# Optimization experiments

Measured on AMD Instinct MI355X. Metric: run time of the kernel, lower is better.

The kernel has to match this reference:

```python
import jax, jax.numpy as jnp
import numpy as np

H = 8        # num_heads
LN_EPS = 1e-5
NEG = -1000000.0


def setup_inputs() -> dict:
    key = jax.random.key(0)
    ks = jax.random.split(key, 8)
    B, T, D = 4, 4096, 1024
    s = 1.0 / np.sqrt(D)
    x = jax.random.normal(ks[0], (B, T, D), dtype=jnp.float32)
    tmask = (jnp.arange(T) < (3 * T) // 4).astype(jnp.float32)
    src_mask = jnp.broadcast_to(tmask[None, :, None], (B, T, 1)).astype(jnp.float32)
    Wq = jax.random.normal(ks[1], (D, D), dtype=jnp.float32) * s
    Wk = jax.random.normal(ks[2], (D, D), dtype=jnp.float32) * s
    Wv = jax.random.normal(ks[3], (D, D), dtype=jnp.float32) * s
    bq = jnp.zeros((D,), jnp.float32)
    bk = jnp.zeros((D,), jnp.float32)
    bv = jnp.zeros((D,), jnp.float32)
    gamma = jnp.ones((D,), jnp.float32)
    beta = jnp.zeros((D,), jnp.float32)
    return {"x": x, "src_mask": src_mask, "Wq": Wq, "bq": bq, "Wk": Wk,
            "bk": bk, "Wv": Wv, "bv": bv, "gamma": gamma, "beta": beta}


def reference(x, src_mask, Wq, bq, Wk, bk, Wv, bv, gamma, beta):
    B, T, D = x.shape
    Dh = D // H
    # LayerNorm (same normed input feeds q, k, v)
    mu = jnp.mean(x, axis=-1, keepdims=True)
    var = jnp.mean(jnp.square(x - mu), axis=-1, keepdims=True)
    xn = (x - mu) * jax.lax.rsqrt(var + LN_EPS) * gamma + beta
    q = xn @ Wq + bq                               # [B,T,D]
    k = xn @ Wk + bk + (1.0 - src_mask) * NEG      # mask padded timesteps
    v = (xn @ Wv + bv) * src_mask                  # zero padded values
    q = jax.nn.softmax(q.reshape(B, T, H, Dh), axis=-1)   # over feature dim
    k = jax.nn.softmax(k.reshape(B, T, H, Dh), axis=1)    # over time dim
    v = v.reshape(B, T, H, Dh)
    # efficient/linear attention: O(T * Dh^2) per head
    att = jnp.einsum('bnhd,bnhl->bhdl', k, v)      # [B,H,Dh,Dh]
    y = jnp.einsum('bnhd,bhdl->bnhl', q, att).reshape(B, T, D)
    return x + y
```

## Files before the change

### kernel.cpp

```cpp
#include <hip/hip_runtime.h>
#include <stdint.h>


typedef unsigned short u16;
typedef __attribute__((ext_vector_type(8))) short bf16x8;
typedef __attribute__((ext_vector_type(4))) float f32x4;

__device__ u16 g_WT[3][1024 * 1024];
__device__ u16 g_xn[16777216];
__device__ u16 g_ekT[16777216];
__device__ u16 g_vvT[16777216];
__device__ float g_attp[8388608];
__device__ u16 g_attT[524288];
__device__ float g_Z[4096];

__device__ __forceinline__ float b2f(u16 u) {
  union { unsigned int i; float f; } c;
  c.i = ((unsigned int)u) << 16;
  return c.f;
}
__device__ __forceinline__ u16 f2b(float f) {
  union { float f; unsigned int i; } c;
  c.f = f;
  unsigned int r = c.i + 0x7fffu + ((c.i >> 16) & 1u);
  return (u16)(r >> 16);
}

__device__ __forceinline__ void gload16(const void* g, void* l) {
  __builtin_amdgcn_global_load_lds(
      reinterpret_cast<const __attribute__((address_space(1))) uint32_t*>(
          reinterpret_cast<uintptr_t>(g)),
      reinterpret_cast<__attribute__((address_space(3))) uint32_t*>(
          reinterpret_cast<uintptr_t>(l)),
      16, 0, 0);
}

__device__ __forceinline__ void stage128x32(const u16* g, int stride, char* lds,
                                            int wave, int lane) {
  const int r = wave * 32 + (lane >> 2);
  const int cb = (lane & 3) * 16;
  const char* gp = (const char*)g;
  gload16(gp + (size_t)r * stride * 2 + cb, lds + wave * 2048);
  gload16(gp + (size_t)(r + 16) * stride * 2 + cb, lds + wave * 2048 + 1024);
}

__device__ __forceinline__ bf16x8 frag_ld(const char* lds, int row, int lane) {
  return *(const bf16x8*)(lds + row * 64 + ((lane >> 4) * 16));
}

__device__ __forceinline__ void tile_mfma(const char* As, const char* Bs,
                                          f32x4 (&acc)[4][4], int wm, int wn,
                                          int lane) {
  bf16x8 af[4], bfr[4];
#pragma unroll
  for (int i = 0; i < 4; i++) af[i] = frag_ld(As, wm * 64 + i * 16 + (lane & 15), lane);
#pragma unroll
  for (int j = 0; j < 4; j++) bfr[j] = frag_ld(Bs, wn * 64 + j * 16 + (lane & 15), lane);
#pragma unroll
  for (int i = 0; i < 4; i++)
#pragma unroll
    for (int j = 0; j < 4; j++)
      acc[i][j] = __builtin_amdgcn_mfma_f32_16x16x32_bf16(af[i], bfr[j], acc[i][j], 0, 0, 0);
}

__device__ __forceinline__ void stageA256(char* buf, const u16* gsrc, int h,
                                          int wave, int lane) {
#pragma unroll
  for (int i = 0; i < 2; i++) {
    const int ib = i * 64 + wave * 8;
    const int rowb = (ib & 63) | ((ib & 64) << 1) | (h << 6);
    const int row = rowb + (lane >> 3);
    const int cc = (lane & 7) ^ (row & 7);
    gload16((const char*)gsrc + ((size_t)row * 1024 + cc * 8) * 2,
            buf + rowb * 128);
  }
}
__device__ __forceinline__ void stageB256(char* buf, const u16* gsrc, int h,
                                          int wave, int lane) {
#pragma unroll
  for (int i = 0; i < 2; i++) {
    const int ib = i * 64 + wave * 8;
    const int rowb = (ib & 31) | ((ib & 96) << 1) | (h << 5);
    const int row = rowb + (lane >> 3);
    const int cc = (lane & 7) ^ (row & 7);
    gload16((const char*)gsrc + ((size_t)row * 1024 + cc * 8) * 2,
            buf + rowb * 128);
  }
}
__device__ __forceinline__ bf16x8 fragS(const char* buf, int R, int ks, int lane) {
  const int q = lane >> 4;
  return *(const bf16x8*)(buf + R * 128 + ((((ks << 2) + q) ^ (R & 7)) << 4));
}

template <bool ST>
__device__ __forceinline__ void tile_r8(char* Ab, char* Bb, char* An, char* Bn,
                                        const u16* Agn, const u16* Bgn,
                                        f32x4 (&acc)[8][4], int wave, int lane,
                                        int wm, int wn) {
  bf16x8 a[4][2], bB[2][2][2];

#pragma unroll
  for (int rf = 0; rf < 4; rf++) {
    const int R = wm * 128 + rf * 16 + (lane & 15);
#pragma unroll
    for (int ks = 0; ks < 2; ks++) a[rf][ks] = fragS(Ab, R, ks, lane);
  }
#pragma unroll
  for (int cf = 0; cf < 2; cf++) {
    const int R = wn * 64 + cf * 16 + (lane & 15);
#pragma unroll
    for (int ks = 0; ks < 2; ks++) bB[0][cf][ks] = fragS(Bb, R, ks, lane);
  }
  if constexpr (ST) {
    stageA256(An, Agn, 0, wave, lane);
    stageB256(Bn, Bgn, 0, wave, lane);
    asm volatile("s_waitcnt vmcnt(4)" ::: "memory");
  } else {
    asm volatile("s_waitcnt vmcnt(0)" ::: "memory");
  }
  __builtin_amdgcn_s_barrier();
  asm volatile("s_waitcnt lgkmcnt(0)" ::: "memory");
  __builtin_amdgcn_sched_barrier(0);
  __builtin_amdgcn_s_setprio(1);
#pragma unroll
  for (int rf = 0; rf < 4; rf++)
#pragma unroll
    for (int cf = 0; cf < 2; cf++)
#pragma unroll
      for (int ks = 0; ks < 2; ks++)
        acc[rf][cf] = __builtin_amdgcn_mfma_f32_16x16x32_bf16(
            a[rf][ks], bB[0][cf][ks], acc[rf][cf], 0, 0, 0);
  __builtin_amdgcn_s_setprio(0);
  __builtin_amdgcn_s_barrier();
  __builtin_amdgcn_sched_barrier(0);

#pragma unroll
  for (int cf = 0; cf < 2; cf++) {
    const int R = wn * 64 + 32 + cf * 16 + (lane & 15);
#pragma unroll
    for (int ks = 0; ks < 2; ks++) bB[1][cf][ks] = fragS(Bb, R, ks, lane);
  }
  if constexpr (ST) stageB256(Bn, Bgn, 1, wave, lane);
  __builtin_amdgcn_s_barrier();
  asm volatile("s_waitcnt lgkmcnt(0)" ::: "memory");
  __builtin_amdgcn_sched_barrier(0);
  __builtin_amdgcn_s_setprio(1);
#pragma unroll
  for (int rf = 0; rf < 4; rf++)
#pragma unroll
    for (int cf = 0; cf < 2; cf++)
#pragma unroll
      for (int ks = 0; ks < 2; ks++)
        acc[rf][2 + cf] = __builtin_amdgcn_mfma_f32_16x16x32_bf16(
            a[rf][ks], bB[1][cf][ks], acc[rf][2 + cf], 0, 0, 0);
  __builtin_amdgcn_s_setprio(0);
  __builtin_amdgcn_s_barrier();
  __builtin_amdgcn_sched_barrier(0);

#pragma unroll
  for (int rf = 0; rf < 4; rf++) {
    const int R = wm * 128 + 64 + rf * 16 + (lane & 15);
#pragma unroll
    for (int ks = 0; ks < 2; ks++) a[rf][ks] = fragS(Ab, R, ks, lane);
  }
  if constexpr (ST) stageA256(An, Agn, 1, wave, lane);
  asm volatile("s_waitcnt vmcnt(4)" ::: "memory");
  __builtin_amdgcn_s_barrier();
  asm volatile("s_waitcnt lgkmcnt(0)" ::: "memory");
  __builtin_amdgcn_sched_barrier(0);
  __builtin_amdgcn_s_setprio(1);
#pragma unroll
  for (int rf = 0; rf < 4; rf++)
#pragma unroll
    for (int cf = 0; cf < 2; cf++)
#pragma unroll
      for (int ks = 0; ks < 2; ks++)
        acc[4 + rf][2 + cf] = __builtin_amdgcn_mfma_f32_16x16x32_bf16(
            a[rf][ks], bB[1][cf][ks], acc[4 + rf][2 + cf], 0, 0, 0);
  __builtin_amdgcn_s_setprio(0);
  __builtin_amdgcn_s_barrier();
  __builtin_amdgcn_sched_barrier(0);

  asm volatile("s_waitcnt vmcnt(2)" ::: "memory");
  __builtin_amdgcn_s_barrier();
  __builtin_amdgcn_s_setprio(1);
#pragma unroll
  for (int rf = 0; rf < 4; rf++)
#pragma unroll
    for (int cf = 0; cf < 2; cf++)
#pragma unroll
      for (int ks = 0; ks < 2; ks++)
        acc[4 + rf][cf] = __builtin_amdgcn_mfma_f32_16x16x32_bf16(
            a[rf][ks], bB[0][cf][ks], acc[4 + rf][cf], 0, 0, 0);
  __builtin_amdgcn_s_setprio(0);
  __builtin_amdgcn_s_barrier();
  __builtin_amdgcn_sched_barrier(0);
}

__global__ __launch_bounds__(256) void prep_kernel(const float* __restrict__ x,
                                                   const float* __restrict__ gamma,
                                                   const float* __restrict__ beta,
                                                   const float* __restrict__ wq,
                                                   const float* __restrict__ wk,
                                                   const float* __restrict__ wv) {
  __shared__ float ls[4], ls2[4];
  __shared__ u16 tile[32][33];
  const int bid = blockIdx.x;
  const int tid = threadIdx.x;
  if (bid < 16384) {
    if (bid < 16) g_Z[bid * 256 + tid] = 0.0f;
    const int wave = tid >> 6, lane = tid & 63;
    const float* xr = x + (size_t)bid * 1024;
    float4 u = ((const float4*)xr)[tid];
    float v0 = u.x, v1 = u.y, v2 = u.z, v3 = u.w;
    float s = v0 + v1 + v2 + v3;
    float s2 = v0 * v0 + v1 * v1 + v2 * v2 + v3 * v3;
#pragma unroll
    for (int off = 32; off > 0; off >>= 1) {
      s += __shfl_down(s, off);
      s2 += __shfl_down(s2, off);
    }
    if (lane == 0) { ls[wave] = s; ls2[wave] = s2; }
    __syncthreads();
    s = ls[0] + ls[1] + ls[2] + ls[3];
    s2 = ls2[0] + ls2[1] + ls2[2] + ls2[3];
    const float mu = s * (1.0f / 1024.0f);
    const float var = fmaxf(s2 * (1.0f / 1024.0f) - mu * mu, 0.0f);
    const float rstd = rsqrtf(var + 1e-5f);
    float4 g4 = ((const float4*)gamma)[tid];
    float4 be = ((const float4*)beta)[tid];
    ushort4 o;
    o.x = f2b((v0 - mu) * rstd * g4.x + be.x);
    o.y = f2b((v1 - mu) * rstd * g4.y + be.y);
    o.z = f2b((v2 - mu) * rstd * g4.z + be.z);
    o.w = f2b((v3 - mu) * rstd * g4.w + be.w);
    *(ushort4*)(g_xn + (size_t)bid * 1024 + tid * 4) = o;
  } else {
    const int id = bid - 16384;
    const int which = id >> 10;
    const int rem = id & 1023;
    const float* src = (which == 0) ? wq : (which == 1) ? wk : wv;
    u16* dst = g_WT[which];
    const int tx = tid & 31;
    const int ty = tid >> 5;
    const int c0 = (rem & 31) * 32, r0 = (rem >> 5) * 32;
#pragma unroll
    for (int i = 0; i < 4; i++)
      tile[ty + i * 8][tx] = f2b(src[(size_t)(r0 + ty + i * 8) * 1024 + c0 + tx]);
    __syncthreads();
#pragma unroll
    for (int i = 0; i < 4; i++)
      dst[(size_t)(c0 + ty + i * 8) * 1024 + r0 + tx] = tile[tx][ty + i * 8];
  }
}

__global__ __launch_bounds__(512, 2) void gemm_kv(const float* __restrict__ bk,
                                                  const float* __restrict__ bv,
                                                  const float* __restrict__ mask) {
  __shared__ __align__(16) char smem[131072];
  const int tid = threadIdx.x, wave = tid >> 6, lane = tid & 63;
  const int L = blockIdx.x;
  const int mt = (L & 7) + 8 * (L >> 6);
  const int nt = (L >> 3) & 7;
  const int n0 = (nt & 3) * 256;
  const int z = nt >> 2;
  const int m0 = mt * 256;
  const u16* wt = z ? g_WT[2] : g_WT[1];
  const float* bias = z ? bv : bk;
  u16* outT = z ? g_vvT : g_ekT;
  const int b = m0 >> 12;
  const int t0 = m0 & 4095;
  const int wm = wave >> 2, wn = wave & 3;
  const u16* Ag = g_xn + (size_t)m0 * 1024;
  const u16* Bg = wt + (size_t)n0 * 1024;

  f32x4 zero = {0.f, 0.f, 0.f, 0.f};
  f32x4 acc[8][4];
#pragma unroll
  for (int i = 0; i < 8; i++)
#pragma unroll
    for (int j = 0; j < 4; j++) acc[i][j] = zero;

  stageA256(smem, Ag, 0, wave, lane);
  stageB256(smem + 65536, Bg, 0, wave, lane);
  stageA256(smem, Ag, 1, wave, lane);
  stageB256(smem + 65536, Bg, 1, wave, lane);
  asm volatile("s_waitcnt vmcnt(0)" ::: "memory");
  __builtin_amdgcn_s_barrier();

#pragma unroll 1
  for (int t = 0; t < 15; ++t) {
    const int p = t & 1;
    tile_r8<true>(smem + p * 32768, smem + 65536 + p * 32768,
                  smem + (p ^ 1) * 32768, smem + 65536 + (p ^ 1) * 32768,
                  Ag + (t + 1) * 64, Bg + (t + 1) * 64, acc, wave, lane, wm, wn);
  }
  tile_r8<false>(smem + 32768, smem + 65536 + 32768, smem, smem + 65536, Ag, Bg,
                 acc, wave, lane, wm, wn);

  u16* tT = (u16*)smem;
  float fsum[4] = {0.f, 0.f, 0.f, 0.f};
#pragma unroll
  for (int rf = 0; rf < 8; rf++)
#pragma unroll
    for (int r = 0; r < 4; r++) {
      const int tok = wm * 128 + rf * 16 + (lane >> 4) * 4 + r;
      const float mv = mask[m0 + tok];
#pragma unroll
      for (int cf = 0; cf < 4; cf++) {
        const int feat = wn * 64 + cf * 16 + (lane & 15);
        const float aV = acc[rf][cf][r] + bias[n0 + feat];
        float o;
        if (z)
          o = aV * mv;
        else
          o = (mv > 0.5f) ? __expf(fminf(aV, 30.0f)) : 0.0f;
        const u16 ob = f2b(o);
        tT[feat * 256 + ((((tok >> 3) ^ (feat & 7)) << 3) | (tok & 7))] = ob;
        if (!z) fsum[cf] += b2f(ob);
      }
    }
  if (!z) {
#pragma unroll
    for (int cf = 0; cf < 4; cf++) {
      float s = fsum[cf];
      s += __shfl_xor(s, 16);
      s += __shfl_xor(s, 32);
      if (lane < 16)
        atomicAdd(&g_Z[b * 1024 + n0 + wn * 64 + cf * 16 + lane], s);
    }
  }
  __syncthreads();
  const size_t gbase = (size_t)b * (1024 * 4096) + (size_t)n0 * 4096 + t0;
#pragma unroll
  for (int u = 0; u < 16; u++) {
    const int id = u * 512 + tid;
    const int feat = id >> 5, c = id & 31;
    uint4 val = *(const uint4*)&tT[feat * 256 + ((c ^ (feat & 7)) << 3)];
    *(uint4*)(outT + gbase + (size_t)feat * 4096 + c * 8) = val;
  }
}

__global__ __launch_bounds__(256) void gemm_att() {
  __shared__ __align__(16) char smem[32768];
  char* A0 = smem;
  char* B0 = smem + 8192;
  char* A1 = smem + 16384;
  char* B1 = smem + 24576;
  const int tid = threadIdx.x, wave = tid >> 6, lane = tid & 63;
  const int kc = blockIdx.x;
  const int bh = blockIdx.y;
  const int b = bh >> 3, h = bh & 7;
  const size_t base = (size_t)b * (1024 * 4096) + (size_t)(h * 128) * 4096;
  const int wm = wave & 1, wn = wave >> 1;
  const u16* Ag = g_ekT + base + kc * 512;
  const u16* Bg = g_vvT + base + kc * 512;

  f32x4 zero = {0.f, 0.f, 0.f, 0.f};
  f32x4 acc[4][4];
#pragma unroll
  for (int i = 0; i < 4; i++)
#pragma unroll
    for (int j = 0; j < 4; j++) acc[i][j] = zero;

  stage128x32(Ag, 4096, A0, wave, lane);
  stage128x32(Bg, 4096, B0, wave, lane);
  __syncthreads();
  for (int kt = 0; kt < 512; kt += 64) {
    stage128x32(Ag + kt + 32, 4096, A1, wave, lane);
    stage128x32(Bg + kt + 32, 4096, B1, wave, lane);
    tile_mfma(A0, B0, acc, wm, wn, lane);
    __syncthreads();
    if (kt + 64 < 512) {
      stage128x32(Ag + kt + 64, 4096, A0, wave, lane);
      stage128x32(Bg + kt + 64, 4096, B0, wave, lane);
    }
    tile_mfma(A1, B1, acc, wm, wn, lane);
    __syncthreads();
  }

  float* op = g_attp + ((size_t)(kc * 32 + bh)) * 16384;
#pragma unroll
  for (int i = 0; i < 4; i++)
#pragma unroll
    for (int r = 0; r < 4; r++) {
      const int row = wm * 64 + i * 16 + (lane >> 4) * 4 + r;
#pragma unroll
      for (int j = 0; j < 4; j++) {
        const int col = wn * 64 + j * 16 + (lane & 15);
        op[row * 128 + col] = acc[i][j][r];
      }
    }
}

__global__ __launch_bounds__(256) void attnorm_kernel() {
  const int bh = blockIdx.x;
  const int b = bh >> 3, h = bh & 7;
  const int tid = threadIdx.x;
  __shared__ float Zl[128];
  if (tid < 128) Zl[tid] = fmaxf(g_Z[b * 1024 + h * 128 + tid], 1e-30f);
  __syncthreads();
  const int i0 = blockIdx.y * 2048;
  for (int i = i0 + tid; i < i0 + 2048; i += 256) {
    const int d = i >> 7, l = i & 127;
    float s = 0.f;
#pragma unroll
    for (int c = 0; c < 8; c++) s += g_attp[((size_t)(c * 32 + bh)) * 16384 + i];
    g_attT[(size_t)bh * 16384 + l * 128 + d] = f2b(s / Zl[d]);
  }
}

__global__ __launch_bounds__(512, 2) void gemm_qy(const float* __restrict__ bq,
                                                  const float* __restrict__ x,
                                                  float* __restrict__ out) {
  __shared__ __align__(16) char smem[131072];
  __shared__ float zq4[4][256];
  const int tid = threadIdx.x, wave = tid >> 6, lane = tid & 63;
  const int L = blockIdx.x;
  const int g = L >> 3;
  const int mt = (L & 7) + 8 * (g >> 2);
  const int n0 = (g & 3) * 256;
  const int m0 = mt * 256;
  const int b = m0 >> 12;
  const int wm = wave >> 2, wn = wave & 3;
  const u16* Ag = g_xn + (size_t)m0 * 1024;
  const u16* Bg = g_WT[0] + (size_t)n0 * 1024;

  f32x4 zero = {0.f, 0.f, 0.f, 0.f};
  f32x4 acc[8][4];
#pragma unroll
  for (int i = 0; i < 8; i++)
#pragma unroll
    for (int j = 0; j < 4; j++) acc[i][j] = zero;

  stageA256(smem, Ag, 0, wave, lane);
  stageB256(smem + 65536, Bg, 0, wave, lane);
  stageA256(smem, Ag, 1, wave, lane);
  stageB256(smem + 65536, Bg, 1, wave, lane);
  asm volatile("s_waitcnt vmcnt(0)" ::: "memory");
  __builtin_amdgcn_s_barrier();

#pragma unroll 1
  for (int t = 0; t < 15; ++t) {
    const int p = t & 1;
    tile_r8<true>(smem + p * 32768, smem + 65536 + p * 32768,
                  smem + (p ^ 1) * 32768, smem + 65536 + (p ^ 1) * 32768,
                  Ag + (t + 1) * 64, Bg + (t + 1) * 64, acc, wave, lane, wm, wn);
  }
  tile_r8<false>(smem + 32768, smem + 65536 + 32768, smem, smem + 65536, Ag, Bg,
                 acc, wave, lane, wm, wn);

  const int hl = wn >> 1;
  const int bhh = b * 8 + (n0 >> 7) + hl;
  const u16* attb = g_attT + ((size_t)bhh << 14);
  bf16x8 bpre[4][4];
#pragma unroll
  for (int ks = 0; ks < 4; ks++)
#pragma unroll
    for (int cf = 0; cf < 4; cf++) {
      const int l = (wn & 1) * 64 + cf * 16 + (lane & 15);
      bpre[ks][cf] = *(const bf16x8*)(attb + l * 128 + ks * 32 + (lane >> 4) * 8);
    }

  u16* qs = (u16*)smem;
#pragma unroll
  for (int rf = 0; rf < 8; rf++)
#pragma unroll
    for (int r = 0; r < 4; r++) {
      const int tok = wm * 128 + rf * 16 + (lane >> 4) * 4 + r;
      float rs = 0.f;
#pragma unroll
      for (int cf = 0; cf < 4; cf++) {
        const int f = wn * 64 + cf * 16 + (lane & 15);
        const float e = __expf(fminf(acc[rf][cf][r] + bq[n0 + f], 30.0f));
        qs[tok * 256 + ((((f >> 3) ^ (tok & 31)) << 3) | (f & 7))] = f2b(e);
        rs += e;
      }
      rs += __shfl_xor(rs, 1);
      rs += __shfl_xor(rs, 2);
      rs += __shfl_xor(rs, 4);
      rs += __shfl_xor(rs, 8);
      if ((lane & 15) == 0) zq4[wn][tok] = rs;
    }
  __syncthreads();

  f32x4 acc2[8][4];
#pragma unroll
  for (int i = 0; i < 8; i++)
#pragma unroll
    for (int j = 0; j < 4; j++) acc2[i][j] = zero;

#pragma unroll
  for (int ks = 0; ks < 4; ks++) {
    bf16x8 af[8];
#pragma unroll
    for (int rf = 0; rf < 8; rf++) {
      const int tok = wm * 128 + rf * 16 + (lane & 15);
      af[rf] = *(const bf16x8*)&qs[tok * 256 +
          ((((hl << 4) + (ks << 2) + (lane >> 4)) ^ (tok & 31)) << 3)];
    }
#pragma unroll
    for (int rf = 0; rf < 8; rf++)
#pragma unroll
      for (int cf = 0; cf < 4; cf++)
        acc2[rf][cf] = __builtin_amdgcn_mfma_f32_16x16x32_bf16(
            af[rf], bpre[ks][cf], acc2[rf][cf], 0, 0, 0);
  }

#pragma unroll
  for (int rf = 0; rf < 8; rf++)
#pragma unroll
    for (int r = 0; r < 4; r++) {
      const int tok = wm * 128 + rf * 16 + (lane >> 4) * 4 + r;
      const float zq =
          fmaxf(zq4[hl * 2][tok] + zq4[hl * 2 + 1][tok], 1e-30f);
      const size_t n = (size_t)(m0 + tok);
#pragma unroll
      for (int cf = 0; cf < 4; cf++) {
        const int f = wn * 64 + cf * 16 + (lane & 15);
        const size_t idx = n * 1024 + n0 + f;
        out[idx] = x[idx] + acc2[rf][cf][r] / zq;
      }
    }
}

extern "C" void kernel_launch(void* const* d_in, const int* in_sizes, int n_in,
                              void* d_out, int out_size, void* d_ws, size_t ws_size,
                              hipStream_t stream) {
  const float* x = (const float*)d_in[0];
  const float* mask = (const float*)d_in[1];
  const float* Wq = (const float*)d_in[2];
  const float* bq = (const float*)d_in[3];
  const float* Wk = (const float*)d_in[4];
  const float* bk = (const float*)d_in[5];
  const float* Wv = (const float*)d_in[6];
  const float* bv = (const float*)d_in[7];
  const float* gamma = (const float*)d_in[8];
  const float* beta = (const float*)d_in[9];
  float* out = (float*)d_out;
  (void)d_ws; (void)ws_size;

  prep_kernel<<<dim3(16384 + 3072), 256, 0, stream>>>(x, gamma, beta, Wq, Wk, Wv);
  gemm_kv<<<dim3(512), 512, 0, stream>>>(bk, bv, mask);
  gemm_att<<<dim3(8, 32), 256, 0, stream>>>();
  attnorm_kernel<<<dim3(32, 8), 256, 0, stream>>>();
  gemm_qy<<<dim3(256), 512, 0, stream>>>(bq, x, out);
}
```

Before: 329.6 us.

## Replace four-phase barriered GEMM tile schedule with single-phase prefetch and one barrier

```diff
diff --git a/kernel.cpp b/kernel.cpp
--- a/kernel.cpp
+++ b/kernel.cpp
@@ -93,106 +93,55 @@
 }
 
 template <bool ST>
-__device__ __forceinline__ void tile_r8(char* Ab, char* Bb, char* An, char* Bn,
-                                        const u16* Agn, const u16* Bgn,
-                                        f32x4 (&acc)[8][4], int wave, int lane,
-                                        int wm, int wn) {
-  bf16x8 a[4][2], bB[2][2][2];
-
+__device__ __forceinline__ void tile_1ph(char* Ab, char* Bb, char* An, char* Bn,
+                                         const u16* Agn, const u16* Bgn,
+                                         f32x4 (&acc)[8][4], int wave, int lane,
+                                         int wm, int wn) {
+  if constexpr (ST) {
+    stageA256(An, Agn, 0, wave, lane);
+    stageA256(An, Agn, 1, wave, lane);
+    stageB256(Bn, Bgn, 0, wave, lane);
+    stageB256(Bn, Bgn, 1, wave, lane);
+  }
+  bf16x8 a[4][2], b[4][2];
+#pragma unroll
+  for (int cf = 0; cf < 4; cf++) {
+    const int R = wn * 64 + cf * 16 + (lane & 15);
+#pragma unroll
+    for (int ks = 0; ks < 2; ks++) b[cf][ks] = fragS(Bb, R, ks, lane);
+  }
 #pragma unroll
   for (int rf = 0; rf < 4; rf++) {
     const int R = wm * 128 + rf * 16 + (lane & 15);
 #pragma unroll
     for (int ks = 0; ks < 2; ks++) a[rf][ks] = fragS(Ab, R, ks, lane);
   }
-#pragma unroll
-  for (int cf = 0; cf < 2; cf++) {
-    const int R = wn * 64 + cf * 16 + (lane & 15);
-#pragma unroll
-    for (int ks = 0; ks < 2; ks++) bB[0][cf][ks] = fragS(Bb, R, ks, lane);
-  }
-  if constexpr (ST) {
-    stageA256(An, Agn, 0, wave, lane);
-    stageB256(Bn, Bgn, 0, wave, lane);
-    asm volatile("s_waitcnt vmcnt(4)" ::: "memory");
-  } else {
-    asm volatile("s_waitcnt vmcnt(0)" ::: "memory");
-  }
-  __builtin_amdgcn_s_barrier();
-  asm volatile("s_waitcnt lgkmcnt(0)" ::: "memory");
-  __builtin_amdgcn_sched_barrier(0);
   __builtin_amdgcn_s_setprio(1);
 #pragma unroll
   for (int rf = 0; rf < 4; rf++)
 #pragma unroll
-    for (int cf = 0; cf < 2; cf++)
+    for (int cf = 0; cf < 4; cf++)
 #pragma unroll
       for (int ks = 0; ks < 2; ks++)
         acc[rf][cf] = __builtin_amdgcn_mfma_f32_16x16x32_bf16(
-            a[rf][ks], bB[0][cf][ks], acc[rf][cf], 0, 0, 0);
-  __builtin_amdgcn_s_setprio(0);
-  __builtin_amdgcn_s_barrier();
-  __builtin_amdgcn_sched_barrier(0);
-
-#pragma unroll
-  for (int cf = 0; cf < 2; cf++) {
-    const int R = wn * 64 + 32 + cf * 16 + (lane & 15);
-#pragma unroll
-    for (int ks = 0; ks < 2; ks++) bB[1][cf][ks] = fragS(Bb, R, ks, lane);
-  }
-  if constexpr (ST) stageB256(Bn, Bgn, 1, wave, lane);
-  __builtin_amdgcn_s_barrier();
-  asm volatile("s_waitcnt lgkmcnt(0)" ::: "memory");
-  __builtin_amdgcn_sched_barrier(0);
-  __builtin_amdgcn_s_setprio(1);
-#pragma unroll
-  for (int rf = 0; rf < 4; rf++)
-#pragma unroll
-    for (int cf = 0; cf < 2; cf++)
-#pragma unroll
-      for (int ks = 0; ks < 2; ks++)
-        acc[rf][2 + cf] = __builtin_amdgcn_mfma_f32_16x16x32_bf16(
-            a[rf][ks], bB[1][cf][ks], acc[rf][2 + cf], 0, 0, 0);
-  __builtin_amdgcn_s_setprio(0);
-  __builtin_amdgcn_s_barrier();
-  __builtin_amdgcn_sched_barrier(0);
-
+            a[rf][ks], b[cf][ks], acc[rf][cf], 0, 0, 0);
+  bf16x8 a2[4][2];
 #pragma unroll
   for (int rf = 0; rf < 4; rf++) {
     const int R = wm * 128 + 64 + rf * 16 + (lane & 15);
 #pragma unroll
-    for (int ks = 0; ks < 2; ks++) a[rf][ks] = fragS(Ab, R, ks, lane);
-  }
-  if constexpr (ST) stageA256(An, Agn, 1, wave, lane);
-  asm volatile("s_waitcnt vmcnt(4)" ::: "memory");
-  __builtin_amdgcn_s_barrier();
-  asm volatile("s_waitcnt lgkmcnt(0)" ::: "memory");
-  __builtin_amdgcn_sched_barrier(0);
-  __builtin_amdgcn_s_setprio(1);
+    for (int ks = 0; ks < 2; ks++) a2[rf][ks] = fragS(Ab, R, ks, lane);
+  }
 #pragma unroll
   for (int rf = 0; rf < 4; rf++)
 #pragma unroll
-    for (int cf = 0; cf < 2; cf++)
-#pragma unroll
-      for (int ks = 0; ks < 2; ks++)
-        acc[4 + rf][2 + cf] = __builtin_amdgcn_mfma_f32_16x16x32_bf16(
-            a[rf][ks], bB[1][cf][ks], acc[4 + rf][2 + cf], 0, 0, 0);
-  __builtin_amdgcn_s_setprio(0);
-  __builtin_amdgcn_s_barrier();
-  __builtin_amdgcn_sched_barrier(0);
-
-  asm volatile("s_waitcnt vmcnt(2)" ::: "memory");
-  __builtin_amdgcn_s_barrier();
-  __builtin_amdgcn_s_setprio(1);
-#pragma unroll
-  for (int rf = 0; rf < 4; rf++)
-#pragma unroll
-    for (int cf = 0; cf < 2; cf++)
+    for (int cf = 0; cf < 4; cf++)
 #pragma unroll
       for (int ks = 0; ks < 2; ks++)
         acc[4 + rf][cf] = __builtin_amdgcn_mfma_f32_16x16x32_bf16(
-            a[rf][ks], bB[0][cf][ks], acc[4 + rf][cf], 0, 0, 0);
+            a2[rf][ks], b[cf][ks], acc[4 + rf][cf], 0, 0, 0);
   __builtin_amdgcn_s_setprio(0);
+  if constexpr (ST) asm volatile("s_waitcnt vmcnt(0)" ::: "memory");
   __builtin_amdgcn_s_barrier();
   __builtin_amdgcn_sched_barrier(0);
 }
@@ -282,8 +231,8 @@
     for (int j = 0; j < 4; j++) acc[i][j] = zero;
 
   stageA256(smem, Ag, 0, wave, lane);
+  stageA256(smem, Ag, 1, wave, lane);
   stageB256(smem + 65536, Bg, 0, wave, lane);
-  stageA256(smem, Ag, 1, wave, lane);
   stageB256(smem + 65536, Bg, 1, wave, lane);
   asm volatile("s_waitcnt vmcnt(0)" ::: "memory");
   __builtin_amdgcn_s_barrier();
@@ -291,12 +240,12 @@
 #pragma unroll 1
   for (int t = 0; t < 15; ++t) {
     const int p = t & 1;
-    tile_r8<true>(smem + p * 32768, smem + 65536 + p * 32768,
-                  smem + (p ^ 1) * 32768, smem + 65536 + (p ^ 1) * 32768,
-                  Ag + (t + 1) * 64, Bg + (t + 1) * 64, acc, wave, lane, wm, wn);
-  }
-  tile_r8<false>(smem + 32768, smem + 65536 + 32768, smem, smem + 65536, Ag, Bg,
-                 acc, wave, lane, wm, wn);
+    tile_1ph<true>(smem + p * 32768, smem + 65536 + p * 32768,
+                   smem + (p ^ 1) * 32768, smem + 65536 + (p ^ 1) * 32768,
+                   Ag + (t + 1) * 64, Bg + (t + 1) * 64, acc, wave, lane, wm, wn);
+  }
+  tile_1ph<false>(smem + 32768, smem + 65536 + 32768, smem, smem + 65536, Ag,
+                  Bg, acc, wave, lane, wm, wn);
 
   u16* tT = (u16*)smem;
   float fsum[4] = {0.f, 0.f, 0.f, 0.f};
@@ -434,8 +383,8 @@
     for (int j = 0; j < 4; j++) acc[i][j] = zero;
 
   stageA256(smem, Ag, 0, wave, lane);
+  stageA256(smem, Ag, 1, wave, lane);
   stageB256(smem + 65536, Bg, 0, wave, lane);
-  stageA256(smem, Ag, 1, wave, lane);
   stageB256(smem + 65536, Bg, 1, wave, lane);
   asm volatile("s_waitcnt vmcnt(0)" ::: "memory");
   __builtin_amdgcn_s_barrier();
@@ -443,12 +392,12 @@
 #pragma unroll 1
   for (int t = 0; t < 15; ++t) {
     const int p = t & 1;
-    tile_r8<true>(smem + p * 32768, smem + 65536 + p * 32768,
-                  smem + (p ^ 1) * 32768, smem + 65536 + (p ^ 1) * 32768,
-                  Ag + (t + 1) * 64, Bg + (t + 1) * 64, acc, wave, lane, wm, wn);
-  }
-  tile_r8<false>(smem + 32768, smem + 65536 + 32768, smem, smem + 65536, Ag, Bg,
-                 acc, wave, lane, wm, wn);
+    tile_1ph<true>(smem + p * 32768, smem + 65536 + p * 32768,
+                   smem + (p ^ 1) * 32768, smem + 65536 + (p ^ 1) * 32768,
+                   Ag + (t + 1) * 64, Bg + (t + 1) * 64, acc, wave, lane, wm, wn);
+  }
+  tile_1ph<false>(smem + 32768, smem + 65536 + 32768, smem, smem + 65536, Ag,
+                  Bg, acc, wave, lane, wm, wn);
 
   const int hl = wn >> 1;
   const int bhh = b * 8 + (n0 >> 7) + hl;
```

After: 331.9 us. Within noise of the previous version (+0.7%).
